# Performance work log

Hardware: AMD Instinct MI355X
Metric: run time of the kernel (lower is better)

Reference implementation:

```python
import jax, jax.numpy as jnp
import numpy as np

TEMPERATURE = 0.2
NUMBER_CLASSES = 1000
LOSS_SCALE = 0.001

N, F = 8192, 256
M = 20000
DEPTH = 4


def setup_inputs() -> dict:
    key = jax.random.key(0)
    k1, k2, k3, k4 = jax.random.split(key, 4)
    gt_labels = jax.random.randint(k1, (N,), 0, NUMBER_CLASSES, dtype=jnp.int32)
    box_features = jax.random.normal(k2, (N, F), dtype=jnp.float32)
    memory = jax.random.normal(k3, (M, F), dtype=jnp.float32)
    trace_idx = jax.random.randint(k4, (NUMBER_CLASSES, DEPTH), 0, M, dtype=jnp.int32)
    return {"gt_labels": gt_labels, "box_features": box_features,
            "memory": memory, "trace_idx": trace_idx}


def reference(gt_labels, box_features, memory, trace_idx):
    # logits[i, j] = dot(f_i, m_j) / T  (the nested python loops fused into one GEMM)
    logits = jnp.einsum('nf,mf->nm', box_features, memory) / TEMPERATURE  # [N, M]
    # fenmu = sum_j exp(logits)  ->  log(fenmu) = logsumexp
    lse = jax.nn.logsumexp(logits, axis=-1)  # [N]
    # gather the trace entries for each item's label: [N, DEPTH]
    traces = trace_idx[gt_labels]  # [N, DEPTH]
    sel = jnp.take_along_axis(logits, traces, axis=1)  # [N, DEPTH]
    depth_w = jnp.arange(DEPTH, dtype=logits.dtype)  # gj = depth
    sum_gj = depth_w.sum()  # sum of layer weights (0+1+2+3)
    # per item: -sum_d gj * log(sim_d / fenmu) / sum_gj
    per_item = -jnp.sum((sel - lse[:, None]) * depth_w, axis=-1) / sum_gj  # [N]
    # background filter: items with label == number_classes contribute nothing
    fg = (gt_labels != NUMBER_CLASSES)
    loss = jnp.sum(jnp.where(fg, per_item, 0.0)) * LOSS_SCALE
    return loss
```

## Files before the change

### kernel.cpp

```cpp
#include <hip/hip_runtime.h>
#include <hip/hip_bf16.h>
#include <stdint.h>

#define NROWS 8192
#define FDIM 256
#define MCOLS 20000
#define NT32 625
#define MSPLIT 8
#define NCLS 1000
#define LOG2E 1.44269504088896f
#define LN2   0.69314718055994f


typedef short short8 __attribute__((ext_vector_type(8)));
typedef float f32x16 __attribute__((ext_vector_type(16)));

__device__ __forceinline__ float ex2(float x) {
    float r;
    asm("v_exp_f32 %0, %1" : "=v"(r) : "v"(x));
    return r;
}

__device__ __forceinline__ unsigned short f2bf(float x) {
    unsigned u = __float_as_uint(x);
    unsigned r = (u + 0x7FFFu + ((u >> 16) & 1u)) >> 16;
    return (unsigned short)r;
}

__device__ __forceinline__ float vmax16(f32x16 v) {
    float x0 = fmaxf(fmaxf(v[0],  v[1]),  v[2]);
    float x1 = fmaxf(fmaxf(v[3],  v[4]),  v[5]);
    float x2 = fmaxf(fmaxf(v[6],  v[7]),  v[8]);
    float x3 = fmaxf(fmaxf(v[9],  v[10]), v[11]);
    float x4 = fmaxf(fmaxf(v[12], v[13]), v[14]);
    float x5 = fmaxf(fmaxf(x0, x1), x2);
    float x6 = fmaxf(fmaxf(x3, x4), v[15]);
    return fmaxf(x5, x6);
}

__global__ void prep_kernel(const float* __restrict__ Mem, unsigned short* __restrict__ Mb2,
                            const float* __restrict__ F, unsigned short* __restrict__ Fb,
                            const int* __restrict__ gt, const int* __restrict__ trace,
                            float* __restrict__ wsel) {
    int b = blockIdx.x;
    if (b < 2500) {
        int g = b * 256 + threadIdx.x;
        int s = g & 63, kk = (g >> 6) & 15, t = g >> 10;
        const float* src = Mem + (size_t)(t * 32 + (s & 31)) * FDIM + kk * 16 + (s >> 5) * 8;
        float4 v0 = ((const float4*)src)[0];
        float4 v1 = ((const float4*)src)[1];
        short8 w;
        w[0] = (short)f2bf(v0.x); w[1] = (short)f2bf(v0.y);
        w[2] = (short)f2bf(v0.z); w[3] = (short)f2bf(v0.w);
        w[4] = (short)f2bf(v1.x); w[5] = (short)f2bf(v1.y);
        w[6] = (short)f2bf(v1.z); w[7] = (short)f2bf(v1.w);
        *(short8*)(Mb2 + (size_t)g * 8) = w;
    } else if (b < 4548) {
        int idx = (b - 2500) * 256 + threadIdx.x;
        float4 v = ((const float4*)F)[idx];
        const float sc = 5.0f * LOG2E;
        ushort4 o;
        o.x = f2bf(v.x * sc); o.y = f2bf(v.y * sc);
        o.z = f2bf(v.z * sc); o.w = f2bf(v.w * sc);
        ((ushort4*)Fb)[idx] = o;
    } else {
        int lane = threadIdx.x & 63, wid = threadIdx.x >> 6;
        int i = (b - 4548) * 4 + wid;
        int label = gt[i];
        float w = 0.0f;
        if (label >= 0 && label < NCLS) {
            float4 fv = ((const float4*)(F + (size_t)i * FDIM))[lane];
            #pragma unroll
            for (int d = 1; d <= 3; ++d) {
                int tr = trace[label * 4 + d];
                float4 mv = ((const float4*)(Mem + (size_t)tr * FDIM))[lane];
                float dot = fv.x*mv.x + fv.y*mv.y + fv.z*mv.z + fv.w*mv.w;
                #pragma unroll
                for (int off = 32; off >= 1; off >>= 1) dot += __shfl_xor(dot, off, 64);
                w += (float)d * dot;
            }
        }
        if (lane == 0) wsel[i] = w * 5.0f;
    }
}

__global__ __attribute__((amdgpu_flat_work_group_size(256, 256), amdgpu_waves_per_eu(1, 1)))
void lse_gemm(
        const unsigned short* __restrict__ Fb, const unsigned short* __restrict__ Mb2,
        float* __restrict__ pm, float* __restrict__ ps) {
    const int split  = blockIdx.x;
    const int rowblk = blockIdx.y;
    const int tid  = threadIdx.x;
    const int lane = tid & 63, wid = tid >> 6;
    const int r0 = lane & 31;
    const int hi = lane >> 5;
    const int rowbase = rowblk * 256 + wid * 64;
    const int l16 = lane << 4;

    short8 al[16], ah[16];
    #pragma unroll
    for (int kk = 0; kk < 16; ++kk) {
        al[kk] = *(const short8*)(Fb + (size_t)(rowbase + r0)      * FDIM + kk * 16 + hi * 8);
        ah[kk] = *(const short8*)(Fb + (size_t)(rowbase + 32 + r0) * FDIM + kk * 16 + hi * 8);
    }

    float m0 = -3.0e38f, s0 = 0.0f, m1 = -3.0e38f, s1 = 0.0f;
    float nmL, nmH, q0, q1, q2, q3, r0x, r1x, r2x, r3x;
    f32x16 accLA, accHA, accLB, accHB;
    short8 b0[16], b1[16];

    const int t0 = (split * NT32) / MSPLIT;
    const int t1 = ((split + 1) * NT32) / MSPLIT;

#define LOADB(BB, t)                                                               \
    do {                                                                           \
        const char* srcT_ = (const char*)Mb2 + (size_t)(t) * 16384 + l16;          \
        _Pragma("unroll")                                                          \
        for (int kk = 0; kk < 16; ++kk)                                            \
            BB[kk] = *(const short8*)(srcT_ + kk * 1024);                          \
    } while (0)

#define MFMA_K(BB, CUR, KK)                                                        \
    {                                                                              \
        accL##CUR = __builtin_amdgcn_mfma_f32_32x32x16_bf16(BB[KK], al[KK], accL##CUR, 0, 0, 0); \
        accH##CUR = __builtin_amdgcn_mfma_f32_32x32x16_bf16(BB[KK], ah[KK], accH##CUR, 0, 0, 0); \
    }

#define SM_P0(P)                                                                   \
    nmL = fmaxf(vmax16(accL##P), m0); nmH = fmaxf(vmax16(accH##P), m1);            \
    q0 = q1 = q2 = q3 = 0.f; r0x = r1x = r2x = r3x = 0.f;

#define SM_P1(P)                                                                   \
    q0 += ex2(accL##P[0] - nmL); q1 += ex2(accL##P[1] - nmL);                      \
    q2 += ex2(accL##P[2] - nmL); q3 += ex2(accL##P[3] - nmL);                      \
    q0 += ex2(accL##P[4] - nmL); q1 += ex2(accL##P[5] - nmL);                      \
    q2 += ex2(accL##P[6] - nmL); q3 += ex2(accL##P[7] - nmL);

#define SM_P2(P)                                                                   \
    q0 += ex2(accL##P[8]  - nmL); q1 += ex2(accL##P[9]  - nmL);                    \
    q2 += ex2(accL##P[10] - nmL); q3 += ex2(accL##P[11] - nmL);                    \
    q0 += ex2(accL##P[12] - nmL); q1 += ex2(accL##P[13] - nmL);                    \
    q2 += ex2(accL##P[14] - nmL); q3 += ex2(accL##P[15] - nmL);                    \
    s0 = fmaf(s0, ex2(m0 - nmL), (q0 + q1) + (q2 + q3)); m0 = nmL;

#define SM_P3(P)                                                                   \
    r0x += ex2(accH##P[0]  - nmH); r1x += ex2(accH##P[1]  - nmH);                  \
    r2x += ex2(accH##P[2]  - nmH); r3x += ex2(accH##P[3]  - nmH);                  \
    r0x += ex2(accH##P[4]  - nmH); r1x += ex2(accH##P[5]  - nmH);                  \
    r2x += ex2(accH##P[6]  - nmH); r3x += ex2(accH##P[7]  - nmH);                  \
    r0x += ex2(accH##P[8]  - nmH); r1x += ex2(accH##P[9]  - nmH);                  \
    r2x += ex2(accH##P[10] - nmH); r3x += ex2(accH##P[11] - nmH);                  \
    r0x += ex2(accH##P[12] - nmH); r1x += ex2(accH##P[13] - nmH);                  \
    r2x += ex2(accH##P[14] - nmH); r3x += ex2(accH##P[15] - nmH);                  \
    s1 = fmaf(s1, ex2(m1 - nmH), (r0x + r1x) + (r2x + r3x)); m1 = nmH;

#define PIPE(BB, CUR, PRV)                                                         \
    do {                                                                           \
        f32x16 z_ = {0,0,0,0,0,0,0,0,0,0,0,0,0,0,0,0};                             \
        accL##CUR = z_; accH##CUR = z_;                                            \
        _Pragma("unroll") for (int kk = 0;  kk < 4;  ++kk) MFMA_K(BB, CUR, kk)     \
        SM_P0(PRV)                                                                 \
        _Pragma("unroll") for (int kk = 4;  kk < 8;  ++kk) MFMA_K(BB, CUR, kk)     \
        SM_P1(PRV)                                                                 \
        _Pragma("unroll") for (int kk = 8;  kk < 12; ++kk) MFMA_K(BB, CUR, kk)     \
        SM_P2(PRV)                                                                 \
        _Pragma("unroll") for (int kk = 12; kk < 16; ++kk) MFMA_K(BB, CUR, kk)     \
        SM_P3(PRV)                                                                 \
    } while (0)

#define MFMA_ONLY(BB, CUR)                                                         \
    do {                                                                           \
        f32x16 z_ = {0,0,0,0,0,0,0,0,0,0,0,0,0,0,0,0};                             \
        accL##CUR = z_; accH##CUR = z_;                                            \
        _Pragma("unroll") for (int kk = 0; kk < 16; ++kk) MFMA_K(BB, CUR, kk)      \
    } while (0)

#define SM_FULL(P) do { SM_P0(P) SM_P1(P) SM_P2(P) SM_P3(P) } while (0)

    LOADB(b0, t0);
    LOADB(b1, t0 + 1);
    MFMA_ONLY(b0, A);

    int t = t0 + 1;
    while (t + 1 < t1) {
        LOADB(b0, t + 1);
        PIPE(b1, B, A);
        if (t + 2 < t1) LOADB(b1, t + 2);
        PIPE(b0, A, B);
        t += 2;
    }
    if (t < t1) {
        PIPE(b1, B, A);
        SM_FULL(B);
    } else {
        SM_FULL(A);
    }

#undef SM_FULL
#undef MFMA_ONLY
#undef PIPE
#undef SM_P3
#undef SM_P2
#undef SM_P1
#undef SM_P0
#undef MFMA_K
#undef LOADB

    {
        float om = __shfl_xor(m0, 32, 64);
        float os = __shfl_xor(s0, 32, 64);
        float nm = fmaxf(m0, om);
        float sf = fmaf(s0, ex2(m0 - nm), os * ex2(om - nm));
        if (lane < 32) {
            pm[split * NROWS + rowbase + lane] = nm;
            ps[split * NROWS + rowbase + lane] = sf;
        }
    }
    {
        float om = __shfl_xor(m1, 32, 64);
        float os = __shfl_xor(s1, 32, 64);
        float nm = fmaxf(m1, om);
        float sf = fmaf(s1, ex2(m1 - nm), os * ex2(om - nm));
        if (lane < 32) {
            pm[split * NROWS + rowbase + 32 + lane] = nm;
            ps[split * NROWS + rowbase + 32 + lane] = sf;
        }
    }
}

__global__ void finalize_kernel(const int* __restrict__ gt, const float* __restrict__ wsel,
                                const float* __restrict__ pm, const float* __restrict__ ps,
                                float* __restrict__ bpart) {
    int tid = threadIdx.x;
    int i = blockIdx.x * 256 + tid;
    float mv[MSPLIT];
    float M = -3.0e38f;
    #pragma unroll
    for (int k = 0; k < MSPLIT; ++k) { mv[k] = pm[k * NROWS + i]; M = fmaxf(M, mv[k]); }
    float S = 0.0f;
    #pragma unroll
    for (int k = 0; k < MSPLIT; ++k) S += ps[k * NROWS + i] * ex2(mv[k] - M);
    float lse = (M + __log2f(S)) * LN2;
    int label = gt[i];
    float per = (label >= 0 && label < NCLS) ? (lse - wsel[i] * (1.0f / 6.0f)) : 0.0f;
    #pragma unroll
    for (int off = 32; off >= 1; off >>= 1) per += __shfl_xor(per, off, 64);
    __shared__ float red[4];
    int lane = tid & 63, wid = tid >> 6;
    if (lane == 0) red[wid] = per;
    __syncthreads();
    if (tid == 0) bpart[blockIdx.x] = red[0] + red[1] + red[2] + red[3];
}

__global__ void sum_kernel(const float* __restrict__ bpart, float* __restrict__ out) {
    int tid = threadIdx.x;
    float v = (tid < 32) ? bpart[tid] : 0.0f;
    #pragma unroll
    for (int off = 32; off >= 1; off >>= 1) v += __shfl_xor(v, off, 64);
    if (tid == 0) out[0] = 0.001f * v;
}

extern "C" void kernel_launch(void* const* d_in, const int* in_sizes, int n_in,
                              void* d_out, int out_size, void* d_ws, size_t ws_size,
                              hipStream_t stream) {
    const int*   gt    = (const int*)d_in[0];
    const float* F     = (const float*)d_in[1];
    const float* Mem   = (const float*)d_in[2];
    const int*   trace = (const int*)d_in[3];
    float* out = (float*)d_out;

    char* w = (char*)d_ws;
    unsigned short* Mb2 = (unsigned short*)w;
    unsigned short* Fb  = (unsigned short*)(w + 10240000);
    float* wsel  = (float*)(w + 14434304);
    float* pm    = (float*)(w + 14467072);
    float* ps    = (float*)(w + 14991360);
    float* bpart = (float*)(w + 15515648);

    prep_kernel<<<dim3(6596), dim3(256), 0, stream>>>(Mem, Mb2, F, Fb, gt, trace, wsel);
    lse_gemm<<<dim3(MSPLIT, NROWS / 256), dim3(256), 0, stream>>>(Fb, Mb2, pm, ps);
    finalize_kernel<<<dim3(NROWS / 256), dim3(256), 0, stream>>>(gt, wsel, pm, ps, bpart);
    sum_kernel<<<dim3(1), dim3(64), 0, stream>>>(bpart, out);
}
```

Before: 96.95 us.

## Double M-splits and replace manual software pipeline with occupancy-based overlap

Doubles the number of column splits so each CU gets two blocks, and raises the kernel to allow two waves per EU via launch bounds. The hand-written double-buffered MFMA/softmax interleaving is replaced by a simple loop. That loop prefetches the next B tile inside the MFMA chain and does the online logsumexp update after each tile. Latency hiding now relies on a second resident wave instead of explicit interleaving. The trade-offs are tighter register pressure and more partial results to merge, and the prefetch reads one tile past the split's end on the last iteration.

```diff
diff --git a/kernel.cpp b/kernel.cpp
--- a/kernel.cpp
+++ b/kernel.cpp
@@ -6,7 +6,7 @@
 #define FDIM 256
 #define MCOLS 20000
 #define NT32 625
-#define MSPLIT 8
+#define MSPLIT 16
 #define NCLS 1000
 #define LOG2E 1.44269504088896f
 #define LN2   0.69314718055994f
@@ -84,8 +84,7 @@
     }
 }
 
-__global__ __attribute__((amdgpu_flat_work_group_size(256, 256), amdgpu_waves_per_eu(1, 1)))
-void lse_gemm(
+__global__ __launch_bounds__(256, 2) void lse_gemm(
         const unsigned short* __restrict__ Fb, const unsigned short* __restrict__ Mb2,
         float* __restrict__ pm, float* __restrict__ ps) {
     const int split  = blockIdx.x;
@@ -105,106 +104,48 @@
     }
 
     float m0 = -3.0e38f, s0 = 0.0f, m1 = -3.0e38f, s1 = 0.0f;
-    float nmL, nmH, q0, q1, q2, q3, r0x, r1x, r2x, r3x;
-    f32x16 accLA, accHA, accLB, accHB;
-    short8 b0[16], b1[16];
 
     const int t0 = (split * NT32) / MSPLIT;
     const int t1 = ((split + 1) * NT32) / MSPLIT;
 
-#define LOADB(BB, t)                                                               \
-    do {                                                                           \
-        const char* srcT_ = (const char*)Mb2 + (size_t)(t) * 16384 + l16;          \
-        _Pragma("unroll")                                                          \
-        for (int kk = 0; kk < 16; ++kk)                                            \
-            BB[kk] = *(const short8*)(srcT_ + kk * 1024);                          \
-    } while (0)
-
-#define MFMA_K(BB, CUR, KK)                                                        \
-    {                                                                              \
-        accL##CUR = __builtin_amdgcn_mfma_f32_32x32x16_bf16(BB[KK], al[KK], accL##CUR, 0, 0, 0); \
-        accH##CUR = __builtin_amdgcn_mfma_f32_32x32x16_bf16(BB[KK], ah[KK], accH##CUR, 0, 0, 0); \
-    }
-
-#define SM_P0(P)                                                                   \
-    nmL = fmaxf(vmax16(accL##P), m0); nmH = fmaxf(vmax16(accH##P), m1);            \
-    q0 = q1 = q2 = q3 = 0.f; r0x = r1x = r2x = r3x = 0.f;
-
-#define SM_P1(P)                                                                   \
-    q0 += ex2(accL##P[0] - nmL); q1 += ex2(accL##P[1] - nmL);                      \
-    q2 += ex2(accL##P[2] - nmL); q3 += ex2(accL##P[3] - nmL);                      \
-    q0 += ex2(accL##P[4] - nmL); q1 += ex2(accL##P[5] - nmL);                      \
-    q2 += ex2(accL##P[6] - nmL); q3 += ex2(accL##P[7] - nmL);
-
-#define SM_P2(P)                                                                   \
-    q0 += ex2(accL##P[8]  - nmL); q1 += ex2(accL##P[9]  - nmL);                    \
-    q2 += ex2(accL##P[10] - nmL); q3 += ex2(accL##P[11] - nmL);                    \
-    q0 += ex2(accL##P[12] - nmL); q1 += ex2(accL##P[13] - nmL);                    \
-    q2 += ex2(accL##P[14] - nmL); q3 += ex2(accL##P[15] - nmL);                    \
-    s0 = fmaf(s0, ex2(m0 - nmL), (q0 + q1) + (q2 + q3)); m0 = nmL;
-
-#define SM_P3(P)                                                                   \
-    r0x += ex2(accH##P[0]  - nmH); r1x += ex2(accH##P[1]  - nmH);                  \
-    r2x += ex2(accH##P[2]  - nmH); r3x += ex2(accH##P[3]  - nmH);                  \
-    r0x += ex2(accH##P[4]  - nmH); r1x += ex2(accH##P[5]  - nmH);                  \
-    r2x += ex2(accH##P[6]  - nmH); r3x += ex2(accH##P[7]  - nmH);                  \
-    r0x += ex2(accH##P[8]  - nmH); r1x += ex2(accH##P[9]  - nmH);                  \
-    r2x += ex2(accH##P[10] - nmH); r3x += ex2(accH##P[11] - nmH);                  \
-    r0x += ex2(accH##P[12] - nmH); r1x += ex2(accH##P[13] - nmH);                  \
-    r2x += ex2(accH##P[14] - nmH); r3x += ex2(accH##P[15] - nmH);                  \
-    s1 = fmaf(s1, ex2(m1 - nmH), (r0x + r1x) + (r2x + r3x)); m1 = nmH;
-
-#define PIPE(BB, CUR, PRV)                                                         \
-    do {                                                                           \
-        f32x16 z_ = {0,0,0,0,0,0,0,0,0,0,0,0,0,0,0,0};                             \
-        accL##CUR = z_; accH##CUR = z_;                                            \
-        _Pragma("unroll") for (int kk = 0;  kk < 4;  ++kk) MFMA_K(BB, CUR, kk)     \
-        SM_P0(PRV)                                                                 \
-        _Pragma("unroll") for (int kk = 4;  kk < 8;  ++kk) MFMA_K(BB, CUR, kk)     \
-        SM_P1(PRV)                                                                 \
-        _Pragma("unroll") for (int kk = 8;  kk < 12; ++kk) MFMA_K(BB, CUR, kk)     \
-        SM_P2(PRV)                                                                 \
-        _Pragma("unroll") for (int kk = 12; kk < 16; ++kk) MFMA_K(BB, CUR, kk)     \
-        SM_P3(PRV)                                                                 \
-    } while (0)
-
-#define MFMA_ONLY(BB, CUR)                                                         \
-    do {                                                                           \
-        f32x16 z_ = {0,0,0,0,0,0,0,0,0,0,0,0,0,0,0,0};                             \
-        accL##CUR = z_; accH##CUR = z_;                                            \
-        _Pragma("unroll") for (int kk = 0; kk < 16; ++kk) MFMA_K(BB, CUR, kk)      \
-    } while (0)
-
-#define SM_FULL(P) do { SM_P0(P) SM_P1(P) SM_P2(P) SM_P3(P) } while (0)
-
-    LOADB(b0, t0);
-    LOADB(b1, t0 + 1);
-    MFMA_ONLY(b0, A);
-
-    int t = t0 + 1;
-    while (t + 1 < t1) {
-        LOADB(b0, t + 1);
-        PIPE(b1, B, A);
-        if (t + 2 < t1) LOADB(b1, t + 2);
-        PIPE(b0, A, B);
-        t += 2;
-    }
-    if (t < t1) {
-        PIPE(b1, B, A);
-        SM_FULL(B);
-    } else {
-        SM_FULL(A);
-    }
-
-#undef SM_FULL
-#undef MFMA_ONLY
-#undef PIPE
-#undef SM_P3
-#undef SM_P2
-#undef SM_P1
-#undef SM_P0
-#undef MFMA_K
-#undef LOADB
+    short8 b[16];
+    {
+        const char* src = (const char*)Mb2 + (size_t)t0 * 16384 + l16;
+        #pragma unroll
+        for (int kk = 0; kk < 16; ++kk)
+            b[kk] = *(const short8*)(src + kk * 1024);
+    }
+
+    for (int t = t0; t < t1; ++t) {
+        const char* nsrc = (const char*)Mb2 + (size_t)(t + 1) * 16384 + l16;
+        f32x16 accL = {0,0,0,0,0,0,0,0,0,0,0,0,0,0,0,0};
+        f32x16 accH = {0,0,0,0,0,0,0,0,0,0,0,0,0,0,0,0};
+        #pragma unroll
+        for (int kk = 0; kk < 16; ++kk) {
+            short8 bb = b[kk];
+            accL = __builtin_amdgcn_mfma_f32_32x32x16_bf16(bb, al[kk], accL, 0, 0, 0);
+            accH = __builtin_amdgcn_mfma_f32_32x32x16_bf16(bb, ah[kk], accH, 0, 0, 0);
+            b[kk] = *(const short8*)(nsrc + kk * 1024);
+        }
+        {
+            float nm = fmaxf(vmax16(accL), m0);
+            float p0 = 0.f, p1 = 0.f;
+            #pragma unroll
+            for (int i = 0; i < 16; i += 2) {
+                p0 += ex2(accL[i] - nm); p1 += ex2(accL[i + 1] - nm);
+            }
+            s0 = fmaf(s0, ex2(m0 - nm), p0 + p1); m0 = nm;
+        }
+        {
+            float nm = fmaxf(vmax16(accH), m1);
+            float p0 = 0.f, p1 = 0.f;
+            #pragma unroll
+            for (int i = 0; i < 16; i += 2) {
+                p0 += ex2(accH[i] - nm); p1 += ex2(accH[i + 1] - nm);
+            }
+            s1 = fmaf(s1, ex2(m1 - nm), p0 + p1); m1 = nm;
+        }
+    }
 
     {
         float om = __shfl_xor(m0, 32, 64);
```

After: 127.0 us. +31.0%, slower.

## Split MFMA accumulators into even/odd chains and interleave softmax with sched barriers

Applied to the files above, without the earlier changes.

Each output tile now accumulates into two independent accumulator sets (even and odd K steps) that are summed before the softmax, breaking the serial MFMA dependency chain. The online softmax of the previous tile is cut into eight smaller slices placed between MFMA pairs, with sched_barrier forcing that interleaving. The aim is to hide MFMA latency and overlap the exp work with matrix ops. The cost is doubled accumulator registers (eight f32x16), which may cut occupancy or cause spills, plus extra vector adds and a fixed schedule the compiler cannot reorder.

```diff
diff --git a/kernel.cpp b/kernel.cpp
--- a/kernel.cpp
+++ b/kernel.cpp
@@ -106,7 +106,7 @@
 
     float m0 = -3.0e38f, s0 = 0.0f, m1 = -3.0e38f, s1 = 0.0f;
     float nmL, nmH, q0, q1, q2, q3, r0x, r1x, r2x, r3x;
-    f32x16 accLA, accHA, accLB, accHB;
+    f32x16 accAL0, accAL1, accAH0, accAH1, accBL0, accBL1, accBH0, accBH1;
     short8 b0[16], b1[16];
 
     const int t0 = (split * NT32) / MSPLIT;
@@ -120,62 +120,69 @@
             BB[kk] = *(const short8*)(srcT_ + kk * 1024);                          \
     } while (0)
 
-#define MFMA_K(BB, CUR, KK)                                                        \
-    {                                                                              \
-        accL##CUR = __builtin_amdgcn_mfma_f32_32x32x16_bf16(BB[KK], al[KK], accL##CUR, 0, 0, 0); \
-        accH##CUR = __builtin_amdgcn_mfma_f32_32x32x16_bf16(BB[KK], ah[KK], accH##CUR, 0, 0, 0); \
-    }
-
-#define SM_P0(P)                                                                   \
-    nmL = fmaxf(vmax16(accL##P), m0); nmH = fmaxf(vmax16(accH##P), m1);            \
-    q0 = q1 = q2 = q3 = 0.f; r0x = r1x = r2x = r3x = 0.f;
-
-#define SM_P1(P)                                                                   \
-    q0 += ex2(accL##P[0] - nmL); q1 += ex2(accL##P[1] - nmL);                      \
-    q2 += ex2(accL##P[2] - nmL); q3 += ex2(accL##P[3] - nmL);                      \
-    q0 += ex2(accL##P[4] - nmL); q1 += ex2(accL##P[5] - nmL);                      \
-    q2 += ex2(accL##P[6] - nmL); q3 += ex2(accL##P[7] - nmL);
-
-#define SM_P2(P)                                                                   \
-    q0 += ex2(accL##P[8]  - nmL); q1 += ex2(accL##P[9]  - nmL);                    \
-    q2 += ex2(accL##P[10] - nmL); q3 += ex2(accL##P[11] - nmL);                    \
-    q0 += ex2(accL##P[12] - nmL); q1 += ex2(accL##P[13] - nmL);                    \
-    q2 += ex2(accL##P[14] - nmL); q3 += ex2(accL##P[15] - nmL);                    \
+#define SB __builtin_amdgcn_sched_barrier(0);
+
+#define MFMA_E(BB, CUR, KK)                                                        \
+    acc##CUR##L0 = __builtin_amdgcn_mfma_f32_32x32x16_bf16(BB[KK], al[KK], acc##CUR##L0, 0, 0, 0); \
+    acc##CUR##H0 = __builtin_amdgcn_mfma_f32_32x32x16_bf16(BB[KK], ah[KK], acc##CUR##H0, 0, 0, 0);
+#define MFMA_O(BB, CUR, KK)                                                        \
+    acc##CUR##L1 = __builtin_amdgcn_mfma_f32_32x32x16_bf16(BB[KK], al[KK], acc##CUR##L1, 0, 0, 0); \
+    acc##CUR##H1 = __builtin_amdgcn_mfma_f32_32x32x16_bf16(BB[KK], ah[KK], acc##CUR##H1, 0, 0, 0);
+
+#define SM0(P) acc##P##L0 = acc##P##L0 + acc##P##L1;
+#define SM1(P) nmL = fmaxf(vmax16(acc##P##L0), m0);              \
+               q0 = q1 = q2 = q3 = 0.f;
+#define SM2(P)                                                                     \
+    q0 += ex2(acc##P##L0[0] - nmL); q1 += ex2(acc##P##L0[1] - nmL);                \
+    q2 += ex2(acc##P##L0[2] - nmL); q3 += ex2(acc##P##L0[3] - nmL);                \
+    q0 += ex2(acc##P##L0[4] - nmL); q1 += ex2(acc##P##L0[5] - nmL);                \
+    q2 += ex2(acc##P##L0[6] - nmL); q3 += ex2(acc##P##L0[7] - nmL);
+#define SM3(P)                                                                     \
+    q0 += ex2(acc##P##L0[8]  - nmL); q1 += ex2(acc##P##L0[9]  - nmL);              \
+    q2 += ex2(acc##P##L0[10] - nmL); q3 += ex2(acc##P##L0[11] - nmL);              \
+    q0 += ex2(acc##P##L0[12] - nmL); q1 += ex2(acc##P##L0[13] - nmL);              \
+    q2 += ex2(acc##P##L0[14] - nmL); q3 += ex2(acc##P##L0[15] - nmL);              \
     s0 = fmaf(s0, ex2(m0 - nmL), (q0 + q1) + (q2 + q3)); m0 = nmL;
-
-#define SM_P3(P)                                                                   \
-    r0x += ex2(accH##P[0]  - nmH); r1x += ex2(accH##P[1]  - nmH);                  \
-    r2x += ex2(accH##P[2]  - nmH); r3x += ex2(accH##P[3]  - nmH);                  \
-    r0x += ex2(accH##P[4]  - nmH); r1x += ex2(accH##P[5]  - nmH);                  \
-    r2x += ex2(accH##P[6]  - nmH); r3x += ex2(accH##P[7]  - nmH);                  \
-    r0x += ex2(accH##P[8]  - nmH); r1x += ex2(accH##P[9]  - nmH);                  \
-    r2x += ex2(accH##P[10] - nmH); r3x += ex2(accH##P[11] - nmH);                  \
-    r0x += ex2(accH##P[12] - nmH); r1x += ex2(accH##P[13] - nmH);                  \
-    r2x += ex2(accH##P[14] - nmH); r3x += ex2(accH##P[15] - nmH);                  \
+#define SM4(P) acc##P##H0 = acc##P##H0 + acc##P##H1;
+#define SM5(P) nmH = fmaxf(vmax16(acc##P##H0), m1);                                \
+               r0x = r1x = r2x = r3x = 0.f;
+#define SM6(P)                                                                     \
+    r0x += ex2(acc##P##H0[0] - nmH); r1x += ex2(acc##P##H0[1] - nmH);              \
+    r2x += ex2(acc##P##H0[2] - nmH); r3x += ex2(acc##P##H0[3] - nmH);              \
+    r0x += ex2(acc##P##H0[4] - nmH); r1x += ex2(acc##P##H0[5] - nmH);              \
+    r2x += ex2(acc##P##H0[6] - nmH); r3x += ex2(acc##P##H0[7] - nmH);
+#define SM7(P)                                                                     \
+    r0x += ex2(acc##P##H0[8]  - nmH); r1x += ex2(acc##P##H0[9]  - nmH);            \
+    r2x += ex2(acc##P##H0[10] - nmH); r3x += ex2(acc##P##H0[11] - nmH);            \
+    r0x += ex2(acc##P##H0[12] - nmH); r1x += ex2(acc##P##H0[13] - nmH);            \
+    r2x += ex2(acc##P##H0[14] - nmH); r3x += ex2(acc##P##H0[15] - nmH);            \
     s1 = fmaf(s1, ex2(m1 - nmH), (r0x + r1x) + (r2x + r3x)); m1 = nmH;
+
+#define ZERO4(CUR)                                                                 \
+    { f32x16 z_ = {0,0,0,0,0,0,0,0,0,0,0,0,0,0,0,0};                               \
+      acc##CUR##L0 = z_; acc##CUR##L1 = z_; acc##CUR##H0 = z_; acc##CUR##H1 = z_; }
 
 #define PIPE(BB, CUR, PRV)                                                         \
     do {                                                                           \
-        f32x16 z_ = {0,0,0,0,0,0,0,0,0,0,0,0,0,0,0,0};                             \
-        accL##CUR = z_; accH##CUR = z_;                                            \
-        _Pragma("unroll") for (int kk = 0;  kk < 4;  ++kk) MFMA_K(BB, CUR, kk)     \
-        SM_P0(PRV)                                                                 \
-        _Pragma("unroll") for (int kk = 4;  kk < 8;  ++kk) MFMA_K(BB, CUR, kk)     \
-        SM_P1(PRV)                                                                 \
-        _Pragma("unroll") for (int kk = 8;  kk < 12; ++kk) MFMA_K(BB, CUR, kk)     \
-        SM_P2(PRV)                                                                 \
-        _Pragma("unroll") for (int kk = 12; kk < 16; ++kk) MFMA_K(BB, CUR, kk)     \
-        SM_P3(PRV)                                                                 \
+        ZERO4(CUR)                                                                 \
+        MFMA_E(BB, CUR, 0)  MFMA_O(BB, CUR, 1)  SM0(PRV) SB                        \
+        MFMA_E(BB, CUR, 2)  MFMA_O(BB, CUR, 3)  SM1(PRV) SB                        \
+        MFMA_E(BB, CUR, 4)  MFMA_O(BB, CUR, 5)  SM2(PRV) SB                        \
+        MFMA_E(BB, CUR, 6)  MFMA_O(BB, CUR, 7)  SM3(PRV) SB                        \
+        MFMA_E(BB, CUR, 8)  MFMA_O(BB, CUR, 9)  SM4(PRV) SB                        \
+        MFMA_E(BB, CUR, 10) MFMA_O(BB, CUR, 11) SM5(PRV) SB                        \
+        MFMA_E(BB, CUR, 12) MFMA_O(BB, CUR, 13) SM6(PRV) SB                        \
+        MFMA_E(BB, CUR, 14) MFMA_O(BB, CUR, 15) SM7(PRV)                           \
     } while (0)
 
 #define MFMA_ONLY(BB, CUR)                                                         \
     do {                                                                           \
-        f32x16 z_ = {0,0,0,0,0,0,0,0,0,0,0,0,0,0,0,0};                             \
-        accL##CUR = z_; accH##CUR = z_;                                            \
-        _Pragma("unroll") for (int kk = 0; kk < 16; ++kk) MFMA_K(BB, CUR, kk)      \
+        ZERO4(CUR)                                                                 \
+        _Pragma("unroll")                                                          \
+        for (int kk = 0; kk < 16; kk += 2) { MFMA_E(BB, CUR, kk) MFMA_O(BB, CUR, kk + 1) } \
     } while (0)
 
-#define SM_FULL(P) do { SM_P0(P) SM_P1(P) SM_P2(P) SM_P3(P) } while (0)
+#define SM_FULL(P) do { SM0(P) SM1(P) SM2(P) SM3(P) SM4(P) SM5(P) SM6(P) SM7(P) } while (0)
 
     LOADB(b0, t0);
     LOADB(b1, t0 + 1);
@@ -199,11 +206,18 @@
 #undef SM_FULL
 #undef MFMA_ONLY
 #undef PIPE
-#undef SM_P3
-#undef SM_P2
-#undef SM_P1
-#undef SM_P0
-#undef MFMA_K
+#undef ZERO4
+#undef SM7
+#undef SM6
+#undef SM5
+#undef SM4
+#undef SM3
+#undef SM2
+#undef SM1
+#undef SM0
+#undef MFMA_O
+#undef MFMA_E
+#undef SB
 #undef LOADB
 
     {
```

After: 108.2 us. +11.6%, slower.
